# Kernel optimization log

Measured on AMD Instinct MI355X. Metric: run time of the kernel, lower is better.

The kernel has to match this reference:

```python
import jax, jax.numpy as jnp
import numpy as np
import math

HIDDEN = 1024
Q_SIZE = 1024
KV_SIZE = 1024
OUT_SIZE = 1024
N_HEADS = 16
D_K = HIDDEN // N_HEADS


def setup_inputs() -> dict:
    key = jax.random.key(0)
    ks = jax.random.split(key, 9)
    b, s, t = 8, 2048, 512
    sc = 0.02
    return {
        "hiddens": jax.random.normal(ks[0], (b, s, KV_SIZE), jnp.float32),
        "query_hiddens": jax.random.normal(ks[1], (b, t, Q_SIZE), jnp.float32),
        "mask": jax.random.randint(ks[2], (b, s), 0, 2, jnp.int32),
        "W_q": jax.random.normal(ks[3], (Q_SIZE, HIDDEN), jnp.float32) * sc,
        "b_q": jnp.zeros((HIDDEN,), jnp.float32),
        "W_k": jax.random.normal(ks[4], (KV_SIZE, HIDDEN), jnp.float32) * sc,
        "W_v": jax.random.normal(ks[5], (KV_SIZE, HIDDEN), jnp.float32) * sc,
        "W_o": jax.random.normal(ks[6], (HIDDEN, OUT_SIZE), jnp.float32) * sc,
        "b_o": jnp.zeros((OUT_SIZE,), jnp.float32),
    }


def reference(hiddens, query_hiddens, mask, W_q, b_q, W_k, W_v, W_o, b_o):
    b, t, _ = query_hiddens.shape
    s = hiddens.shape[1]
    # projections (dropout p=0 in eval -> identity)
    Q = (query_hiddens @ W_q + b_q).reshape(b, t, N_HEADS, D_K)
    K = (hiddens @ W_k).reshape(b, s, N_HEADS, D_K)
    V = (hiddens @ W_v).reshape(b, s, N_HEADS, D_K)
    # scores: [b, t, s, h] matching e = (Q*K).sum(-1)/sqrt(d_k)
    e = jnp.einsum('bthd,bshd->btsh', Q, K) / math.sqrt(D_K)
    neg = (1.0 - mask.astype(e.dtype)) * (-1e20)  # [b, s]
    e = e + neg[:, None, :, None]
    a = jax.nn.softmax(e, axis=2)  # softmax over seqlen
    concat = jnp.einsum('btsh,bshd->bthd', a, V).reshape(b, t, HIDDEN)
    context = concat @ W_o + b_o
    return context, a.mean(axis=-1)
```

## Files before the change

kernel.cpp:

```cpp
#include <hip/hip_runtime.h>
#include <hip/hip_bf16.h>

using short8  = __attribute__((ext_vector_type(8))) short;
using short4v = __attribute__((ext_vector_type(4))) short;
using f32x4   = __attribute__((ext_vector_type(4))) float;

#define LSK 72

#define GLDS(gptr, lptr) __builtin_amdgcn_global_load_lds( \
    (const __attribute__((address_space(1))) void*)(gptr), \
    (__attribute__((address_space(3))) void*)(lptr), 16, 0, 0)

#define GLDS4(gptr, lptr) __builtin_amdgcn_global_load_lds( \
    (const __attribute__((address_space(1))) void*)(gptr), \
    (__attribute__((address_space(3))) void*)(lptr), 4, 0, 0)

#define TOPSYNC_V(n_lit) do { \
    asm volatile("s_waitcnt vmcnt(" #n_lit ")" ::: "memory"); \
    __builtin_amdgcn_s_barrier(); \
    __builtin_amdgcn_sched_barrier(0); \
} while (0)
#define ENDSYNC() do { \
    __builtin_amdgcn_sched_barrier(0); \
    __builtin_amdgcn_s_barrier(); \
} while (0)

static __device__ __forceinline__ short f2b(float f) {
    unsigned u = __builtin_bit_cast(unsigned, f);
    unsigned r = (u + 0x7fffu + ((u >> 16) & 1u)) >> 16;
    return (short)r;
}

__global__ void cvt_bf16(const float* __restrict__ in, short* __restrict__ out, int n) {
    int i = (blockIdx.x * 256 + threadIdx.x) * 4;
    if (i >= n) return;
    float4 v = *(const float4*)(in + i);
    short4 o = make_short4(f2b(v.x), f2b(v.y), f2b(v.z), f2b(v.w));
    *(short4*)(out + i) = o;
}

__global__ void cvt_t4(const float* __restrict__ W0, const float* __restrict__ W1,
                       const float* __restrict__ W2, const float* __restrict__ W3,
                       short* __restrict__ Wt0) {
    __shared__ short tile[32][33];
    const float* Ws[4] = {W0, W1, W2, W3};
    const float* W = Ws[blockIdx.z];
    short* Wt = Wt0 + (size_t)blockIdx.z * 1024 * 1024;
    const int K = 1024, N = 1024;
    int n0 = blockIdx.x * 32, k0 = blockIdx.y * 32;
    int tx = threadIdx.x, ty = threadIdx.y;
#pragma unroll
    for (int i = 0; i < 4; i++) {
        int r = ty + i * 8;
        tile[r][tx] = f2b(W[(size_t)(k0 + r) * N + n0 + tx]);
    }
    __syncthreads();
#pragma unroll
    for (int i = 0; i < 4; i++) {
        int r = ty + i * 8;
        Wt[(size_t)(n0 + r) * K + k0 + tx] = tile[tx][r];
    }
}

__global__ __launch_bounds__(512, 1) void gemm256(
    const short* __restrict__ A, const short* __restrict__ Bt,
    short* __restrict__ CK, short* __restrict__ CVt)
{
    __shared__ short lds[65536];
    const int tid = threadIdx.x;
    const int w = tid >> 6, L = tid & 63, quad = L >> 4, l16 = L & 15;
    const int wr = w >> 2, wcn = w & 3;

    const int lin = blockIdx.y * gridDim.x + blockIdx.x;
    const int xcd = lin & 7, idx = lin >> 3;
    const int mPer = gridDim.y >> 3;
    const int my = xcd * mPer + idx / gridDim.x;
    const int nx = idx % gridDim.x;
    const int n0 = nx * 256, m0 = my * 256;

    const int K = 1024;
    const int srow_in = L >> 3;
    const int sgcol   = ((L & 7) ^ srow_in) * 8;

    auto STAGE_ALL = [&](int buf, int kt) {
        const int k0 = kt * 64;
#pragma unroll
        for (int j = 0; j < 8; j++) {
            int c = w * 8 + j;
            if (c < 32) {
                int row = c * 8 + srow_in;
                GLDS(A + (size_t)(m0 + row) * K + k0 + sgcol, &lds[buf * 16384 + c * 512]);
            } else {
                int row = (c - 32) * 8 + srow_in;
                GLDS(Bt + (size_t)(n0 + row) * K + k0 + sgcol, &lds[32768 + buf * 16384 + (c - 32) * 512]);
            }
        }
    };

    f32x4 acc[2][4][4];
#pragma unroll
    for (int mh = 0; mh < 2; mh++)
#pragma unroll
        for (int mi = 0; mi < 4; mi++)
#pragma unroll
            for (int ni = 0; ni < 4; ni++) acc[mh][mi][ni] = (f32x4){0.f, 0.f, 0.f, 0.f};

    STAGE_ALL(0, 0);

    for (int t = 0; t < 16; t++) {
        const int cur = t & 1;
        if (t < 15) {
            STAGE_ALL(cur ^ 1, t + 1);
            TOPSYNC_V(8);
        } else {
            TOPSYNC_V(0);
        }
#pragma unroll
        for (int ks = 0; ks < 2; ks++) {
            const int swz = (((ks * 4) + quad) ^ (l16 & 7)) << 3;
            short8 bf[4];
#pragma unroll
            for (int ni = 0; ni < 4; ni++)
                bf[ni] = *(const short8*)&lds[32768 + cur * 16384 + (wcn * 64 + ni * 16 + l16) * 64 + swz];
#pragma unroll
            for (int mh = 0; mh < 2; mh++) {
                short8 af[4];
#pragma unroll
                for (int mi = 0; mi < 4; mi++)
                    af[mi] = *(const short8*)&lds[cur * 16384 + (wr * 128 + mh * 64 + mi * 16 + l16) * 64 + swz];
                __builtin_amdgcn_s_setprio(1);
#pragma unroll
                for (int mi = 0; mi < 4; mi++)
#pragma unroll
                    for (int ni = 0; ni < 4; ni++)
                        acc[mh][mi][ni] = __builtin_amdgcn_mfma_f32_16x16x32_bf16(af[mi], bf[ni], acc[mh][mi][ni], 0, 0, 0);
                __builtin_amdgcn_s_setprio(0);
            }
        }
        ENDSYNC();
    }

    if (n0 < 1024) {
#pragma unroll
        for (int mh = 0; mh < 2; mh++)
#pragma unroll
            for (int ni = 0; ni < 4; ni++) {
                int n = n0 + wcn * 64 + ni * 16 + l16;
#pragma unroll
                for (int mi = 0; mi < 4; mi++)
#pragma unroll
                    for (int r = 0; r < 4; r++) {
                        int m = m0 + wr * 128 + mh * 64 + mi * 16 + quad * 4 + r;
                        CK[(size_t)m * 1024 + n] = f2b(acc[mh][mi][ni][r]);
                    }
            }
    } else {
#pragma unroll
        for (int mh = 0; mh < 2; mh++)
#pragma unroll
            for (int mi = 0; mi < 4; mi++) {
                const int g = wr * 32 + mh * 16 + mi * 4 + quad;
#pragma unroll
                for (int ni = 0; ni < 4; ni++) {
                    int n = wcn * 64 + ni * 16 + l16;
                    short4v v;
#pragma unroll
                    for (int r = 0; r < 4; r++) v[r] = f2b(acc[mh][mi][ni][r]);
                    *(short4v*)&lds[n * 256 + ((g ^ (n & 15)) << 2)] = v;
                }
            }
        __syncthreads();
        const int hb = (n0 - 1024) >> 6;
        const int bb = m0 >> 11, sb = m0 & 2047;
#pragma unroll
        for (int i = 0; i < 16; i++) {
            int row = w * 32 + i * 2 + (L >> 5);
            int cg  = (L & 31) * 2;
            int sw  = row & 15;
            short4v a = *(const short4v*)&lds[row * 256 + ((cg ^ sw) << 2)];
            short4v c2 = *(const short4v*)&lds[row * 256 + (((cg + 1) ^ sw) << 2)];
            short8 o;
            o[0] = a[0]; o[1] = a[1]; o[2] = a[2]; o[3] = a[3];
            o[4] = c2[0]; o[5] = c2[1]; o[6] = c2[2]; o[7] = c2[3];
            int h = hb + (row >> 6), d = row & 63;
            *(short8*)&CVt[(((size_t)bb * 16 + h) * 64 + d) * 2048 + sb + (L & 31) * 8] = o;
        }
    }
}

__global__ __launch_bounds__(256) void gemm128(
    const short* __restrict__ A, const short* __restrict__ Bt,
    const float* __restrict__ bias, void* __restrict__ Cout,
    int M, int mode)
{
    __shared__ short As[2][128 * 64];
    __shared__ short Bs[2][128 * 64];
    const int tid = threadIdx.x;
    const int w = tid >> 6, L = tid & 63, quad = L >> 4, l16 = L & 15;
    const int wr = w >> 1, wc = w & 1;

    const int lin = blockIdx.y * gridDim.x + blockIdx.x;
    const int xcd = lin & 7, idx = lin >> 3;
    const int mPer = gridDim.y >> 3;
    const int my = xcd * mPer + idx / gridDim.x;
    const int nx = idx % gridDim.x;
    const int n0 = nx * 128, m0 = my * 128;

    const int K = 1024;
    const int srow_in = L >> 3;
    const int sgcol   = ((L & 7) ^ (srow_in & 7)) * 8;

    auto STAGE = [&](int buf, int k0) {
#pragma unroll
        for (int j = 0; j < 8; j++) {
            int c = w * 8 + j;
            if (c < 16) {
                int row = c * 8 + srow_in;
                GLDS(A + (size_t)(m0 + row) * K + k0 + sgcol, &As[buf][c * 512]);
            } else {
                int row = (c - 16) * 8 + srow_in;
                GLDS(Bt + (size_t)(n0 + row) * K + k0 + sgcol, &Bs[buf][(c - 16) * 512]);
            }
        }
    };

    f32x4 acc[4][4];
#pragma unroll
    for (int mi = 0; mi < 4; mi++)
#pragma unroll
        for (int ni = 0; ni < 4; ni++) acc[mi][ni] = (f32x4){0.f, 0.f, 0.f, 0.f};

    STAGE(0, 0);

    for (int t = 0; t < 16; t++) {
        const int cur = t & 1;
        if (t < 15) {
            STAGE(cur ^ 1, (t + 1) * 64);
            TOPSYNC_V(8);
        } else {
            TOPSYNC_V(0);
        }
#pragma unroll
        for (int kk = 0; kk < 64; kk += 32) {
            const int swz = (((kk >> 3) + quad) ^ (l16 & 7)) << 3;
            short8 af[4], bf[4];
#pragma unroll
            for (int mi = 0; mi < 4; mi++)
                af[mi] = *(const short8*)&As[cur][(wr * 64 + mi * 16 + l16) * 64 + swz];
#pragma unroll
            for (int ni = 0; ni < 4; ni++)
                bf[ni] = *(const short8*)&Bs[cur][(wc * 64 + ni * 16 + l16) * 64 + swz];
#pragma unroll
            for (int mi = 0; mi < 4; mi++)
#pragma unroll
                for (int ni = 0; ni < 4; ni++)
                    acc[mi][ni] = __builtin_amdgcn_mfma_f32_16x16x32_bf16(af[mi], bf[ni], acc[mi][ni], 0, 0, 0);
        }
        ENDSYNC();
    }

#pragma unroll
    for (int ni = 0; ni < 4; ni++) {
        int n = n0 + wc * 64 + ni * 16 + l16;
        float bv = bias ? bias[n] : 0.f;
#pragma unroll
        for (int mi = 0; mi < 4; mi++) {
#pragma unroll
            for (int r = 0; r < 4; r++) {
                int m = m0 + wr * 64 + mi * 16 + quad * 4 + r;
                float v = acc[mi][ni][r] + bv;
                if (mode == 1)      ((float*)Cout)[(size_t)m * 1024 + n] = v;
                else                ((short*)Cout)[(size_t)m * 1024 + n] = f2b(v);
            }
        }
    }
}

__global__ __launch_bounds__(512) void attn_flash(
    const short* __restrict__ Qb, const short* __restrict__ Kb, const short* __restrict__ Vtb,
    const int* __restrict__ mask, short* __restrict__ Cb, float* __restrict__ lse)
{
    __shared__ short Qs[128 * 64];
    __shared__ short Ks[2][128 * 64];
    __shared__ short Vts[2][128 * 64];
    __shared__ short Ps[128 * LSK];
    __shared__ int   negi[2048];
    const int tid = threadIdx.x;
    const int w = tid >> 6, L = tid & 63, quad = L >> 4, l16 = L & 15;
    const int t0 = blockIdx.x * 128, h = blockIdx.y, b = blockIdx.z;
    const int S = 2048, T = 512, H = 1024;
    const int trow = w * 16;
    const int srow = L >> 3;
    const int sg   = ((L & 7) ^ srow) * 8;

    auto STAGE_KV = [&](int buf, int s0) {
#pragma unroll
        for (int j = 0; j < 2; j++) {
            int krow = w * 16 + j * 8 + srow;
            GLDS(Kb + ((size_t)b * S + s0 + krow) * H + h * 64 + sg, &Ks[buf][(w * 16 + j * 8) * 64]);
            int c = w * 2 + j, hf = c >> 3, d0 = (c & 7) * 8;
            GLDS(Vtb + (((size_t)b * 16 + h) * 64 + d0 + srow) * S + s0 + hf * 64 + sg, &Vts[buf][c * 512]);
        }
    };

#pragma unroll
    for (int j = 0; j < 2; j++) {
        int row = w * 16 + j * 8 + srow;
        GLDS(Qb + ((size_t)b * T + t0 + row) * H + h * 64 + sg, &Qs[(w * 16 + j * 8) * 64]);
    }
#pragma unroll
    for (int r = 0; r < 4; r++)
        GLDS4(mask + (size_t)b * S + r * 512 + w * 64 + L, &negi[r * 512 + w * 64]);
    STAGE_KV(0, 0);
    __syncthreads();

    short8 aq[2];
#pragma unroll
    for (int kk = 0; kk < 2; kk++)
        aq[kk] = *(const short8*)&Qs[(trow + l16) * 64 + ((kk * 4 + quad) ^ (l16 & 7)) * 8];

    f32x4 Oacc[4];
#pragma unroll
    for (int nt = 0; nt < 4; nt++) Oacc[nt] = (f32x4){0.f, 0.f, 0.f, 0.f};
    float lsum[4] = {0.f, 0.f, 0.f, 0.f};

    for (int it = 0; it < 16; it++) {
        const int cur = it & 1;
        if (it < 15) {
            STAGE_KV(cur ^ 1, (it + 1) * 128);
            TOPSYNC_V(4);
        } else {
            TOPSYNC_V(0);
        }
#pragma unroll
        for (int hf = 0; hf < 2; hf++) {
            f32x4 sacc[4];
#pragma unroll
            for (int nt = 0; nt < 4; nt++) sacc[nt] = (f32x4){0.f, 0.f, 0.f, 0.f};
#pragma unroll
            for (int kk = 0; kk < 2; kk++) {
#pragma unroll
                for (int nt = 0; nt < 4; nt++) {
                    short8 bf = *(const short8*)&Ks[cur][(hf * 64 + nt * 16 + l16) * 64 + ((kk * 4 + quad) ^ (l16 & 7)) * 8];
                    sacc[nt] = __builtin_amdgcn_mfma_f32_16x16x32_bf16(aq[kk], bf, sacc[nt], 0, 0, 0);
                }
            }
#pragma unroll
            for (int nt = 0; nt < 4; nt++) {
                float ng = negi[it * 128 + hf * 64 + nt * 16 + l16] ? 0.f : -1e20f;
#pragma unroll
                for (int r = 0; r < 4; r++) {
                    float e = __expf(fmaf(sacc[nt][r], 0.125f, ng));
                    lsum[r] += e;
                    Ps[(trow + quad * 4 + r) * LSK + nt * 16 + l16] = f2b(e);
                }
            }
#pragma unroll
            for (int kk = 0; kk < 2; kk++) {
                short8 af = *(const short8*)&Ps[(trow + l16) * LSK + kk * 32 + quad * 8];
#pragma unroll
                for (int nt = 0; nt < 4; nt++) {
                    short8 bf = *(const short8*)&Vts[cur][hf * 4096 + (nt * 16 + l16) * 64 + ((kk * 4 + quad) ^ (l16 & 7)) * 8];
                    Oacc[nt] = __builtin_amdgcn_mfma_f32_16x16x32_bf16(af, bf, Oacc[nt], 0, 0, 0);
                }
            }
        }
        ENDSYNC();
    }
#pragma unroll
    for (int r = 0; r < 4; r++) {
#pragma unroll
        for (int off = 1; off < 16; off <<= 1)
            lsum[r] += __shfl_xor(lsum[r], off, 64);
    }
#pragma unroll
    for (int r = 0; r < 4; r++) {
        float inv = 1.0f / lsum[r];
        int t = t0 + trow + quad * 4 + r;
#pragma unroll
        for (int nt = 0; nt < 4; nt++) {
            int d = nt * 16 + l16;
            Cb[((size_t)b * T + t) * H + h * 64 + d] = f2b(Oacc[nt][r] * inv);
        }
        if (l16 == 0)
            lse[((size_t)b * 16 + h) * T + t] = __logf(lsum[r]);
    }
}

__global__ __launch_bounds__(256) void attn_amean(
    const short* __restrict__ Qb, const short* __restrict__ Kb,
    const int* __restrict__ mask, const float* __restrict__ lse, float* __restrict__ outA)
{
    __shared__ short Qs[2][64 * 64];
    __shared__ short Ks[2][64 * 64];
    __shared__ float neg[64];
    __shared__ float lss[16 * 64];
    const int tid = threadIdx.x;
    const int w = tid >> 6, L = tid & 63, quad = L >> 4, l16 = L & 15;
    const int s0 = blockIdx.x * 64, t0 = blockIdx.y * 64, b = blockIdx.z;
    const int S = 2048, T = 512, H = 1024;
    const int srow = L >> 3;
    const int sg   = ((L & 7) ^ srow) * 8;

    auto STAGE_QK = [&](int buf, int h) {
#pragma unroll
        for (int j = 0; j < 2; j++) {
            int row = w * 16 + j * 8 + srow;
            GLDS(Qb + ((size_t)b * T + t0 + row) * H + h * 64 + sg, &Qs[buf][(w * 16 + j * 8) * 64]);
            GLDS(Kb + ((size_t)b * S + s0 + row) * H + h * 64 + sg, &Ks[buf][(w * 16 + j * 8) * 64]);
        }
    };

    if (tid < 64) neg[tid] = mask[(size_t)b * S + s0 + tid] ? 0.f : -1e20f;
    for (int i = tid; i < 16 * 64; i += 256) {
        int hh = i >> 6, tt = i & 63;
        lss[i] = lse[((size_t)b * 16 + hh) * T + t0 + tt];
    }
    STAGE_QK(0, 0);
    __syncthreads();

    float am[4][4] = {};
    for (int h = 0; h < 16; h++) {
        const int cur = h & 1;
        if (h < 15) {
            STAGE_QK(cur ^ 1, h + 1);
            TOPSYNC_V(4);
        } else {
            TOPSYNC_V(0);
        }
        short8 aq[2];
#pragma unroll
        for (int kk = 0; kk < 2; kk++)
            aq[kk] = *(const short8*)&Qs[cur][(w * 16 + l16) * 64 + ((kk * 4 + quad) ^ (l16 & 7)) * 8];
        f32x4 sacc[4];
#pragma unroll
        for (int nt = 0; nt < 4; nt++) sacc[nt] = (f32x4){0.f, 0.f, 0.f, 0.f};
#pragma unroll
        for (int kk = 0; kk < 2; kk++) {
#pragma unroll
            for (int nt = 0; nt < 4; nt++) {
                short8 bf = *(const short8*)&Ks[cur][(nt * 16 + l16) * 64 + ((kk * 4 + quad) ^ (l16 & 7)) * 8];
                sacc[nt] = __builtin_amdgcn_mfma_f32_16x16x32_bf16(aq[kk], bf, sacc[nt], 0, 0, 0);
            }
        }
#pragma unroll
        for (int nt = 0; nt < 4; nt++) {
            float ng = neg[nt * 16 + l16];
#pragma unroll
            for (int r = 0; r < 4; r++) {
                int trow = w * 16 + quad * 4 + r;
                am[nt][r] += __expf(fmaf(sacc[nt][r], 0.125f, ng - lss[h * 64 + trow]));
            }
        }
        ENDSYNC();
    }
#pragma unroll
    for (int r = 0; r < 4; r++) {
        int t = t0 + w * 16 + quad * 4 + r;
#pragma unroll
        for (int nt = 0; nt < 4; nt++) {
            int s = s0 + nt * 16 + l16;
            outA[((size_t)b * T + t) * S + s] = am[nt][r] * 0.0625f;
        }
    }
}

extern "C" void kernel_launch(void* const* d_in, const int* in_sizes, int n_in,
                              void* d_out, int out_size, void* d_ws, size_t ws_size,
                              hipStream_t stream) {
    const float* hiddens = (const float*)d_in[0];
    const float* query   = (const float*)d_in[1];
    const int*   mask    = (const int*)d_in[2];
    const float* W_q = (const float*)d_in[3];
    const float* b_q = (const float*)d_in[4];
    const float* W_k = (const float*)d_in[5];
    const float* W_v = (const float*)d_in[6];
    const float* W_o = (const float*)d_in[7];
    const float* b_o = (const float*)d_in[8];
    float* out = (float*)d_out;

    constexpr size_t N_H  = 8UL * 2048 * 1024;
    constexpr size_t N_QH = 8UL * 512 * 1024;
    constexpr size_t N_W  = 1024UL * 1024;
    char* ws = (char*)d_ws;
    short* Hb   = (short*)(ws);
    short* QHb  = (short*)(ws + N_H * 2);
    short* Wqt  = (short*)(ws + N_H * 2 + N_QH * 2);
    short* Wkt  = Wqt + N_W;
    short* Wvt  = Wkt + N_W;
    short* Wot  = Wvt + N_W;
    short* Qb   = Wot + N_W;
    short* Kb   = Qb + N_QH;
    short* Vtb  = Kb + N_H;
    short* Cb   = Vtb + N_H;
    float* lseP = (float*)(Cb + N_QH);

    cvt_bf16<<<16384, 256, 0, stream>>>(hiddens, Hb, (int)N_H);
    cvt_bf16<<<4096, 256, 0, stream>>>(query, QHb, (int)N_QH);
    cvt_t4<<<dim3(32, 32, 4), dim3(32, 8), 0, stream>>>(W_q, W_k, W_v, W_o, Wqt);

    gemm128<<<dim3(8, 32), 256, 0, stream>>>(QHb, Wqt, b_q, Qb, 4096, 0);
    gemm256<<<dim3(8, 64), 512, 0, stream>>>(Hb, Wkt, Kb, Vtb);

    attn_flash<<<dim3(4, 16, 8), 512, 0, stream>>>(Qb, Kb, Vtb, mask, Cb, lseP);

    gemm128<<<dim3(8, 32), 256, 0, stream>>>(Cb, Wot, b_o, out, 4096, 1);
    attn_amean<<<dim3(32, 8, 8), 256, 0, stream>>>(Qb, Kb, mask, lseP, out + N_QH);
}
```

Before: 387.1 us.

## Enlarge attention tiles to reuse K/V fragments across more query rows

attn_flash now gives each block 256 query rows instead of 128. Each warp handles two 16-row m-tiles, so every K and V fragment read from LDS feeds two MFMAs, and the grid halves. attn_amean moves from 64x64 to 128x128 tiles with 512 threads, and each warp computes eight column tiles per Q fragment. The goal is fewer redundant global and LDS loads of Q/K/V per output. The cost is higher LDS use and register pressure, and fewer blocks to fill the GPU.

```diff
diff --git a/kernel.cpp b/kernel.cpp
--- a/kernel.cpp
+++ b/kernel.cpp
@@ -280,16 +280,16 @@
     const short* __restrict__ Qb, const short* __restrict__ Kb, const short* __restrict__ Vtb,
     const int* __restrict__ mask, short* __restrict__ Cb, float* __restrict__ lse)
 {
-    __shared__ short Qs[128 * 64];
+    __shared__ short Qs[256 * 64];
     __shared__ short Ks[2][128 * 64];
     __shared__ short Vts[2][128 * 64];
-    __shared__ short Ps[128 * LSK];
+    __shared__ short Ps[256 * LSK];
     __shared__ int   negi[2048];
     const int tid = threadIdx.x;
     const int w = tid >> 6, L = tid & 63, quad = L >> 4, l16 = L & 15;
-    const int t0 = blockIdx.x * 128, h = blockIdx.y, b = blockIdx.z;
+    const int t0 = blockIdx.x * 256, h = blockIdx.y, b = blockIdx.z;
     const int S = 2048, T = 512, H = 1024;
-    const int trow = w * 16;
+    const int trow = w * 32;
     const int srow = L >> 3;
     const int sg   = ((L & 7) ^ srow) * 8;
 
@@ -304,9 +304,9 @@
     };
 
 #pragma unroll
-    for (int j = 0; j < 2; j++) {
-        int row = w * 16 + j * 8 + srow;
-        GLDS(Qb + ((size_t)b * T + t0 + row) * H + h * 64 + sg, &Qs[(w * 16 + j * 8) * 64]);
+    for (int j = 0; j < 4; j++) {
+        int row = w * 32 + j * 8 + srow;
+        GLDS(Qb + ((size_t)b * T + t0 + row) * H + h * 64 + sg, &Qs[(w * 32 + j * 8) * 64]);
     }
 #pragma unroll
     for (int r = 0; r < 4; r++)
@@ -314,15 +314,19 @@
     STAGE_KV(0, 0);
     __syncthreads();
 
-    short8 aq[2];
-#pragma unroll
-    for (int kk = 0; kk < 2; kk++)
-        aq[kk] = *(const short8*)&Qs[(trow + l16) * 64 + ((kk * 4 + quad) ^ (l16 & 7)) * 8];
-
-    f32x4 Oacc[4];
-#pragma unroll
-    for (int nt = 0; nt < 4; nt++) Oacc[nt] = (f32x4){0.f, 0.f, 0.f, 0.f};
-    float lsum[4] = {0.f, 0.f, 0.f, 0.f};
+    short8 aq[2][2];
+#pragma unroll
+    for (int mt = 0; mt < 2; mt++)
+#pragma unroll
+        for (int kk = 0; kk < 2; kk++)
+            aq[mt][kk] = *(const short8*)&Qs[(trow + mt * 16 + l16) * 64 + ((kk * 4 + quad) ^ (l16 & 7)) * 8];
+
+    f32x4 Oacc[2][4];
+#pragma unroll
+    for (int mt = 0; mt < 2; mt++)
+#pragma unroll
+        for (int nt = 0; nt < 4; nt++) Oacc[mt][nt] = (f32x4){0.f, 0.f, 0.f, 0.f};
+    float lsum[2][4] = {};
 
     for (int it = 0; it < 16; it++) {
         const int cur = it & 1;
@@ -334,70 +338,85 @@
         }
 #pragma unroll
         for (int hf = 0; hf < 2; hf++) {
-            f32x4 sacc[4];
-#pragma unroll
-            for (int nt = 0; nt < 4; nt++) sacc[nt] = (f32x4){0.f, 0.f, 0.f, 0.f};
+            f32x4 sacc[2][4];
+#pragma unroll
+            for (int mt = 0; mt < 2; mt++)
+#pragma unroll
+                for (int nt = 0; nt < 4; nt++) sacc[mt][nt] = (f32x4){0.f, 0.f, 0.f, 0.f};
 #pragma unroll
             for (int kk = 0; kk < 2; kk++) {
 #pragma unroll
                 for (int nt = 0; nt < 4; nt++) {
                     short8 bf = *(const short8*)&Ks[cur][(hf * 64 + nt * 16 + l16) * 64 + ((kk * 4 + quad) ^ (l16 & 7)) * 8];
-                    sacc[nt] = __builtin_amdgcn_mfma_f32_16x16x32_bf16(aq[kk], bf, sacc[nt], 0, 0, 0);
+#pragma unroll
+                    for (int mt = 0; mt < 2; mt++)
+                        sacc[mt][nt] = __builtin_amdgcn_mfma_f32_16x16x32_bf16(aq[mt][kk], bf, sacc[mt][nt], 0, 0, 0);
                 }
             }
 #pragma unroll
-            for (int nt = 0; nt < 4; nt++) {
-                float ng = negi[it * 128 + hf * 64 + nt * 16 + l16] ? 0.f : -1e20f;
-#pragma unroll
-                for (int r = 0; r < 4; r++) {
-                    float e = __expf(fmaf(sacc[nt][r], 0.125f, ng));
-                    lsum[r] += e;
-                    Ps[(trow + quad * 4 + r) * LSK + nt * 16 + l16] = f2b(e);
+            for (int mt = 0; mt < 2; mt++)
+#pragma unroll
+                for (int nt = 0; nt < 4; nt++) {
+                    float ng = negi[it * 128 + hf * 64 + nt * 16 + l16] ? 0.f : -1e20f;
+#pragma unroll
+                    for (int r = 0; r < 4; r++) {
+                        float e = __expf(fmaf(sacc[mt][nt][r], 0.125f, ng));
+                        lsum[mt][r] += e;
+                        Ps[(trow + mt * 16 + quad * 4 + r) * LSK + nt * 16 + l16] = f2b(e);
+                    }
                 }
-            }
 #pragma unroll
             for (int kk = 0; kk < 2; kk++) {
-                short8 af = *(const short8*)&Ps[(trow + l16) * LSK + kk * 32 + quad * 8];
+                short8 af[2];
+#pragma unroll
+                for (int mt = 0; mt < 2; mt++)
+                    af[mt] = *(const short8*)&Ps[(trow + mt * 16 + l16) * LSK + kk * 32 + quad * 8];
 #pragma unroll
                 for (int nt = 0; nt < 4; nt++) {
                     short8 bf = *(const short8*)&Vts[cur][hf * 4096 + (nt * 16 + l16) * 64 + ((kk * 4 + quad) ^ (l16 & 7)) * 8];
-                    Oacc[nt] = __builtin_amdgcn_mfma_f32_16x16x32_bf16(af, bf, Oacc[nt], 0, 0, 0);
+#pragma unroll
+                    for (int mt = 0; mt < 2; mt++)
+                        Oacc[mt][nt] = __builtin_amdgcn_mfma_f32_16x16x32_bf16(af[mt], bf, Oacc[mt][nt], 0, 0, 0);
                 }
             }
         }
         ENDSYNC();
     }
 #pragma unroll
-    for (int r = 0; r < 4; r++) {
-#pragma unroll
-        for (int off = 1; off < 16; off <<= 1)
-            lsum[r] += __shfl_xor(lsum[r], off, 64);
-    }
-#pragma unroll
-    for (int r = 0; r < 4; r++) {
-        float inv = 1.0f / lsum[r];
-        int t = t0 + trow + quad * 4 + r;
-#pragma unroll
-        for (int nt = 0; nt < 4; nt++) {
-            int d = nt * 16 + l16;
-            Cb[((size_t)b * T + t) * H + h * 64 + d] = f2b(Oacc[nt][r] * inv);
-        }
-        if (l16 == 0)
-            lse[((size_t)b * 16 + h) * T + t] = __logf(lsum[r]);
-    }
-}
-
-__global__ __launch_bounds__(256) void attn_amean(
+    for (int mt = 0; mt < 2; mt++)
+#pragma unroll
+        for (int r = 0; r < 4; r++) {
+#pragma unroll
+            for (int off = 1; off < 16; off <<= 1)
+                lsum[mt][r] += __shfl_xor(lsum[mt][r], off, 64);
+        }
+#pragma unroll
+    for (int mt = 0; mt < 2; mt++)
+#pragma unroll
+        for (int r = 0; r < 4; r++) {
+            float inv = 1.0f / lsum[mt][r];
+            int t = t0 + trow + mt * 16 + quad * 4 + r;
+#pragma unroll
+            for (int nt = 0; nt < 4; nt++) {
+                int d = nt * 16 + l16;
+                Cb[((size_t)b * T + t) * H + h * 64 + d] = f2b(Oacc[mt][nt][r] * inv);
+            }
+            if (l16 == 0)
+                lse[((size_t)b * 16 + h) * T + t] = __logf(lsum[mt][r]);
+        }
+}
+
+__global__ __launch_bounds__(512) void attn_amean(
     const short* __restrict__ Qb, const short* __restrict__ Kb,
     const int* __restrict__ mask, const float* __restrict__ lse, float* __restrict__ outA)
 {
-    __shared__ short Qs[2][64 * 64];
-    __shared__ short Ks[2][64 * 64];
-    __shared__ float neg[64];
-    __shared__ float lss[16 * 64];
+    __shared__ short Qs[2][128 * 64];
+    __shared__ short Ks[2][128 * 64];
+    __shared__ float neg[128];
+    __shared__ float lss[16 * 128];
     const int tid = threadIdx.x;
     const int w = tid >> 6, L = tid & 63, quad = L >> 4, l16 = L & 15;
-    const int s0 = blockIdx.x * 64, t0 = blockIdx.y * 64, b = blockIdx.z;
+    const int s0 = blockIdx.x * 128, t0 = blockIdx.y * 128, b = blockIdx.z;
     const int S = 2048, T = 512, H = 1024;
     const int srow = L >> 3;
     const int sg   = ((L & 7) ^ srow) * 8;
@@ -411,15 +430,15 @@
         }
     };
 
-    if (tid < 64) neg[tid] = mask[(size_t)b * S + s0 + tid] ? 0.f : -1e20f;
-    for (int i = tid; i < 16 * 64; i += 256) {
-        int hh = i >> 6, tt = i & 63;
+    if (tid < 128) neg[tid] = mask[(size_t)b * S + s0 + tid] ? 0.f : -1e20f;
+    for (int i = tid; i < 16 * 128; i += 512) {
+        int hh = i >> 7, tt = i & 127;
         lss[i] = lse[((size_t)b * 16 + hh) * T + t0 + tt];
     }
     STAGE_QK(0, 0);
     __syncthreads();
 
-    float am[4][4] = {};
+    float am[8][4] = {};
     for (int h = 0; h < 16; h++) {
         const int cur = h & 1;
         if (h < 15) {
@@ -432,24 +451,24 @@
 #pragma unroll
         for (int kk = 0; kk < 2; kk++)
             aq[kk] = *(const short8*)&Qs[cur][(w * 16 + l16) * 64 + ((kk * 4 + quad) ^ (l16 & 7)) * 8];
-        f32x4 sacc[4];
-#pragma unroll
-        for (int nt = 0; nt < 4; nt++) sacc[nt] = (f32x4){0.f, 0.f, 0.f, 0.f};
+        f32x4 sacc[8];
+#pragma unroll
+        for (int nt = 0; nt < 8; nt++) sacc[nt] = (f32x4){0.f, 0.f, 0.f, 0.f};
 #pragma unroll
         for (int kk = 0; kk < 2; kk++) {
 #pragma unroll
-            for (int nt = 0; nt < 4; nt++) {
+            for (int nt = 0; nt < 8; nt++) {
                 short8 bf = *(const short8*)&Ks[cur][(nt * 16 + l16) * 64 + ((kk * 4 + quad) ^ (l16 & 7)) * 8];
                 sacc[nt] = __builtin_amdgcn_mfma_f32_16x16x32_bf16(aq[kk], bf, sacc[nt], 0, 0, 0);
             }
         }
 #pragma unroll
-        for (int nt = 0; nt < 4; nt++) {
+        for (int nt = 0; nt < 8; nt++) {
             float ng = neg[nt * 16 + l16];
 #pragma unroll
             for (int r = 0; r < 4; r++) {
                 int trow = w * 16 + quad * 4 + r;
-                am[nt][r] += __expf(fmaf(sacc[nt][r], 0.125f, ng - lss[h * 64 + trow]));
+                am[nt][r] += __expf(fmaf(sacc[nt][r], 0.125f, ng - lss[h * 128 + trow]));
             }
         }
         ENDSYNC();
@@ -458,7 +477,7 @@
     for (int r = 0; r < 4; r++) {
         int t = t0 + w * 16 + quad * 4 + r;
 #pragma unroll
-        for (int nt = 0; nt < 4; nt++) {
+        for (int nt = 0; nt < 8; nt++) {
             int s = s0 + nt * 16 + l16;
             outA[((size_t)b * T + t) * S + s] = am[nt][r] * 0.0625f;
         }
@@ -502,8 +521,8 @@
     gemm128<<<dim3(8, 32), 256, 0, stream>>>(QHb, Wqt, b_q, Qb, 4096, 0);
     gemm256<<<dim3(8, 64), 512, 0, stream>>>(Hb, Wkt, Kb, Vtb);
 
-    attn_flash<<<dim3(4, 16, 8), 512, 0, stream>>>(Qb, Kb, Vtb, mask, Cb, lseP);
+    attn_flash<<<dim3(2, 16, 8), 512, 0, stream>>>(Qb, Kb, Vtb, mask, Cb, lseP);
 
     gemm128<<<dim3(8, 32), 256, 0, stream>>>(Cb, Wot, b_o, out, 4096, 1);
-    attn_amean<<<dim3(32, 8, 8), 256, 0, stream>>>(Qb, Kb, mask, lseP, out + N_QH);
-}
+    attn_amean<<<dim3(16, 4, 8), 512, 0, stream>>>(Qb, Kb, mask, lseP, out + N_QH);
+}
```

New measurement: 373.7 us. 1.04x faster.

## Shrink flash KV tile and share Q/P LDS; enlarge attention-mean tile

Applied to the files above, without the earlier changes.

The flash-attention kernel now streams K/V in 64-row tiles instead of 128, and reuses one LDS buffer for both Q and P. Q is pulled into registers before the loop, with a wait so the buffer can then be overwritten by P. This cuts shared-memory use, and a launch-bounds hint asks for more resident blocks per CU, in exchange for twice as many loop iterations and barriers. The attention-mean kernel moves from 64x64 tiles with 256 threads to 128x128 tiles with 512 threads. That improves Q/K reuse per staged load, but needs more registers and LDS per block and launches fewer blocks.

```diff
diff --git a/kernel.cpp b/kernel.cpp
--- a/kernel.cpp
+++ b/kernel.cpp
@@ -276,14 +276,13 @@
     }
 }
 
-__global__ __launch_bounds__(512) void attn_flash(
+__global__ __launch_bounds__(512, 4) void attn_flash(
     const short* __restrict__ Qb, const short* __restrict__ Kb, const short* __restrict__ Vtb,
     const int* __restrict__ mask, short* __restrict__ Cb, float* __restrict__ lse)
 {
-    __shared__ short Qs[128 * 64];
-    __shared__ short Ks[2][128 * 64];
-    __shared__ short Vts[2][128 * 64];
-    __shared__ short Ps[128 * LSK];
+    __shared__ short QPs[128 * LSK];
+    __shared__ short Ks[2][64 * 64];
+    __shared__ short Vts[2][64 * 64];
     __shared__ int   negi[2048];
     const int tid = threadIdx.x;
     const int w = tid >> 6, L = tid & 63, quad = L >> 4, l16 = L & 15;
@@ -294,19 +293,14 @@
     const int sg   = ((L & 7) ^ srow) * 8;
 
     auto STAGE_KV = [&](int buf, int s0) {
-#pragma unroll
-        for (int j = 0; j < 2; j++) {
-            int krow = w * 16 + j * 8 + srow;
-            GLDS(Kb + ((size_t)b * S + s0 + krow) * H + h * 64 + sg, &Ks[buf][(w * 16 + j * 8) * 64]);
-            int c = w * 2 + j, hf = c >> 3, d0 = (c & 7) * 8;
-            GLDS(Vtb + (((size_t)b * 16 + h) * 64 + d0 + srow) * S + s0 + hf * 64 + sg, &Vts[buf][c * 512]);
-        }
+        GLDS(Kb + ((size_t)b * S + s0 + w * 8 + srow) * H + h * 64 + sg, &Ks[buf][w * 512]);
+        GLDS(Vtb + (((size_t)b * 16 + h) * 64 + w * 8 + srow) * S + s0 + sg, &Vts[buf][w * 512]);
     };
 
 #pragma unroll
     for (int j = 0; j < 2; j++) {
         int row = w * 16 + j * 8 + srow;
-        GLDS(Qb + ((size_t)b * T + t0 + row) * H + h * 64 + sg, &Qs[(w * 16 + j * 8) * 64]);
+        GLDS(Qb + ((size_t)b * T + t0 + row) * H + h * 64 + sg, &QPs[(w * 16 + j * 8) * 64]);
     }
 #pragma unroll
     for (int r = 0; r < 4; r++)
@@ -317,52 +311,50 @@
     short8 aq[2];
 #pragma unroll
     for (int kk = 0; kk < 2; kk++)
-        aq[kk] = *(const short8*)&Qs[(trow + l16) * 64 + ((kk * 4 + quad) ^ (l16 & 7)) * 8];
+        aq[kk] = *(const short8*)&QPs[(trow + l16) * 64 + ((kk * 4 + quad) ^ (l16 & 7)) * 8];
+    asm volatile("s_waitcnt lgkmcnt(0)" ::: "memory");
 
     f32x4 Oacc[4];
 #pragma unroll
     for (int nt = 0; nt < 4; nt++) Oacc[nt] = (f32x4){0.f, 0.f, 0.f, 0.f};
     float lsum[4] = {0.f, 0.f, 0.f, 0.f};
 
-    for (int it = 0; it < 16; it++) {
+    for (int it = 0; it < 32; it++) {
         const int cur = it & 1;
-        if (it < 15) {
-            STAGE_KV(cur ^ 1, (it + 1) * 128);
-            TOPSYNC_V(4);
+        if (it < 31) {
+            STAGE_KV(cur ^ 1, (it + 1) * 64);
+            TOPSYNC_V(2);
         } else {
             TOPSYNC_V(0);
         }
-#pragma unroll
-        for (int hf = 0; hf < 2; hf++) {
-            f32x4 sacc[4];
-#pragma unroll
-            for (int nt = 0; nt < 4; nt++) sacc[nt] = (f32x4){0.f, 0.f, 0.f, 0.f};
-#pragma unroll
-            for (int kk = 0; kk < 2; kk++) {
-#pragma unroll
-                for (int nt = 0; nt < 4; nt++) {
-                    short8 bf = *(const short8*)&Ks[cur][(hf * 64 + nt * 16 + l16) * 64 + ((kk * 4 + quad) ^ (l16 & 7)) * 8];
-                    sacc[nt] = __builtin_amdgcn_mfma_f32_16x16x32_bf16(aq[kk], bf, sacc[nt], 0, 0, 0);
-                }
-            }
+        f32x4 sacc[4];
+#pragma unroll
+        for (int nt = 0; nt < 4; nt++) sacc[nt] = (f32x4){0.f, 0.f, 0.f, 0.f};
+#pragma unroll
+        for (int kk = 0; kk < 2; kk++) {
 #pragma unroll
             for (int nt = 0; nt < 4; nt++) {
-                float ng = negi[it * 128 + hf * 64 + nt * 16 + l16] ? 0.f : -1e20f;
-#pragma unroll
-                for (int r = 0; r < 4; r++) {
-                    float e = __expf(fmaf(sacc[nt][r], 0.125f, ng));
-                    lsum[r] += e;
-                    Ps[(trow + quad * 4 + r) * LSK + nt * 16 + l16] = f2b(e);
-                }
-            }
-#pragma unroll
-            for (int kk = 0; kk < 2; kk++) {
-                short8 af = *(const short8*)&Ps[(trow + l16) * LSK + kk * 32 + quad * 8];
-#pragma unroll
-                for (int nt = 0; nt < 4; nt++) {
-                    short8 bf = *(const short8*)&Vts[cur][hf * 4096 + (nt * 16 + l16) * 64 + ((kk * 4 + quad) ^ (l16 & 7)) * 8];
-                    Oacc[nt] = __builtin_amdgcn_mfma_f32_16x16x32_bf16(af, bf, Oacc[nt], 0, 0, 0);
-                }
+                short8 bf = *(const short8*)&Ks[cur][(nt * 16 + l16) * 64 + ((kk * 4 + quad) ^ (l16 & 7)) * 8];
+                sacc[nt] = __builtin_amdgcn_mfma_f32_16x16x32_bf16(aq[kk], bf, sacc[nt], 0, 0, 0);
+            }
+        }
+#pragma unroll
+        for (int nt = 0; nt < 4; nt++) {
+            float ng = negi[it * 64 + nt * 16 + l16] ? 0.f : -1e20f;
+#pragma unroll
+            for (int r = 0; r < 4; r++) {
+                float e = __expf(fmaf(sacc[nt][r], 0.125f, ng));
+                lsum[r] += e;
+                QPs[(trow + quad * 4 + r) * LSK + nt * 16 + l16] = f2b(e);
+            }
+        }
+#pragma unroll
+        for (int kk = 0; kk < 2; kk++) {
+            short8 af = *(const short8*)&QPs[(trow + l16) * LSK + kk * 32 + quad * 8];
+#pragma unroll
+            for (int nt = 0; nt < 4; nt++) {
+                short8 bf = *(const short8*)&Vts[cur][(nt * 16 + l16) * 64 + ((kk * 4 + quad) ^ (l16 & 7)) * 8];
+                Oacc[nt] = __builtin_amdgcn_mfma_f32_16x16x32_bf16(af, bf, Oacc[nt], 0, 0, 0);
             }
         }
         ENDSYNC();
@@ -387,17 +379,17 @@
     }
 }
 
-__global__ __launch_bounds__(256) void attn_amean(
+__global__ __launch_bounds__(512) void attn_amean(
     const short* __restrict__ Qb, const short* __restrict__ Kb,
     const int* __restrict__ mask, const float* __restrict__ lse, float* __restrict__ outA)
 {
-    __shared__ short Qs[2][64 * 64];
-    __shared__ short Ks[2][64 * 64];
-    __shared__ float neg[64];
-    __shared__ float lss[16 * 64];
+    __shared__ short Qs[2][128 * 64];
+    __shared__ short Ks[2][128 * 64];
+    __shared__ float neg[128];
+    __shared__ float lss[16 * 128];
     const int tid = threadIdx.x;
     const int w = tid >> 6, L = tid & 63, quad = L >> 4, l16 = L & 15;
-    const int s0 = blockIdx.x * 64, t0 = blockIdx.y * 64, b = blockIdx.z;
+    const int s0 = blockIdx.x * 128, t0 = blockIdx.y * 128, b = blockIdx.z;
     const int S = 2048, T = 512, H = 1024;
     const int srow = L >> 3;
     const int sg   = ((L & 7) ^ srow) * 8;
@@ -411,15 +403,15 @@
         }
     };
 
-    if (tid < 64) neg[tid] = mask[(size_t)b * S + s0 + tid] ? 0.f : -1e20f;
-    for (int i = tid; i < 16 * 64; i += 256) {
-        int hh = i >> 6, tt = i & 63;
+    if (tid < 128) neg[tid] = mask[(size_t)b * S + s0 + tid] ? 0.f : -1e20f;
+    for (int i = tid; i < 16 * 128; i += 512) {
+        int hh = i >> 7, tt = i & 127;
         lss[i] = lse[((size_t)b * 16 + hh) * T + t0 + tt];
     }
     STAGE_QK(0, 0);
     __syncthreads();
 
-    float am[4][4] = {};
+    float am[8][4] = {};
     for (int h = 0; h < 16; h++) {
         const int cur = h & 1;
         if (h < 15) {
@@ -432,24 +424,24 @@
 #pragma unroll
         for (int kk = 0; kk < 2; kk++)
             aq[kk] = *(const short8*)&Qs[cur][(w * 16 + l16) * 64 + ((kk * 4 + quad) ^ (l16 & 7)) * 8];
-        f32x4 sacc[4];
-#pragma unroll
-        for (int nt = 0; nt < 4; nt++) sacc[nt] = (f32x4){0.f, 0.f, 0.f, 0.f};
+        f32x4 sacc[8];
+#pragma unroll
+        for (int nt = 0; nt < 8; nt++) sacc[nt] = (f32x4){0.f, 0.f, 0.f, 0.f};
 #pragma unroll
         for (int kk = 0; kk < 2; kk++) {
 #pragma unroll
-            for (int nt = 0; nt < 4; nt++) {
+            for (int nt = 0; nt < 8; nt++) {
                 short8 bf = *(const short8*)&Ks[cur][(nt * 16 + l16) * 64 + ((kk * 4 + quad) ^ (l16 & 7)) * 8];
                 sacc[nt] = __builtin_amdgcn_mfma_f32_16x16x32_bf16(aq[kk], bf, sacc[nt], 0, 0, 0);
             }
         }
 #pragma unroll
-        for (int nt = 0; nt < 4; nt++) {
+        for (int nt = 0; nt < 8; nt++) {
             float ng = neg[nt * 16 + l16];
 #pragma unroll
             for (int r = 0; r < 4; r++) {
                 int trow = w * 16 + quad * 4 + r;
-                am[nt][r] += __expf(fmaf(sacc[nt][r], 0.125f, ng - lss[h * 64 + trow]));
+                am[nt][r] += __expf(fmaf(sacc[nt][r], 0.125f, ng - lss[h * 128 + trow]));
             }
         }
         ENDSYNC();
@@ -458,7 +450,7 @@
     for (int r = 0; r < 4; r++) {
         int t = t0 + w * 16 + quad * 4 + r;
 #pragma unroll
-        for (int nt = 0; nt < 4; nt++) {
+        for (int nt = 0; nt < 8; nt++) {
             int s = s0 + nt * 16 + l16;
             outA[((size_t)b * T + t) * S + s] = am[nt][r] * 0.0625f;
         }
@@ -505,5 +497,5 @@
     attn_flash<<<dim3(4, 16, 8), 512, 0, stream>>>(Qb, Kb, Vtb, mask, Cb, lseP);
 
     gemm128<<<dim3(8, 32), 256, 0, stream>>>(Cb, Wot, b_o, out, 4096, 1);
-    attn_amean<<<dim3(32, 8, 8), 256, 0, stream>>>(Qb, Kb, mask, lseP, out + N_QH);
-}
+    attn_amean<<<dim3(16, 4, 8), 512, 0, stream>>>(Qb, Kb, mask, lseP, out + N_QH);
+}
```

New measurement: 367.4 us. 1.05x faster.
